# Performance work log

Hardware: AMD Instinct MI355X
Metric: run time of the kernel (lower is better)

## Reference

```python
import jax, jax.numpy as jnp
import numpy as np

N_NODES = 20000
N_EDGES = 320000
MUL = 64            # multiplicity of 0e and 1o in hidden/out irreps
NUM_BASIS = 8
INV_SQRT3 = 0.5773502691896258
EPS = 1e-5


def setup_inputs() -> dict:
    key = jax.random.key(0)
    k = jax.random.split(key, 16)
    return {
        "node_hiddens": jax.random.normal(k[0], (N_NODES, 4 * MUL), dtype=jnp.float32),
        "edge_attr": jax.random.uniform(k[1], (N_EDGES, NUM_BASIS), dtype=jnp.float32),
        "edge_sh": jax.random.normal(k[2], (N_EDGES, 4), dtype=jnp.float32),
        "w1_s": jax.random.normal(k[3], (MUL, MUL), dtype=jnp.float32),
        "w1_v": jax.random.normal(k[4], (MUL, MUL), dtype=jnp.float32),
        "wsc_s": jax.random.normal(k[5], (MUL, MUL), dtype=jnp.float32),
        "wsc_v": jax.random.normal(k[6], (MUL, MUL), dtype=jnp.float32),
        "w2_s": jax.random.normal(k[7], (2 * MUL, MUL), dtype=jnp.float32),
        "w2_v": jax.random.normal(k[8], (2 * MUL, MUL), dtype=jnp.float32),
        "fc_w1": jax.random.normal(k[9], (NUM_BASIS, 64), dtype=jnp.float32),
        "fc_w2": jax.random.normal(k[10], (64, 64), dtype=jnp.float32),
        "fc_w3": jax.random.normal(k[11], (64, 4 * MUL), dtype=jnp.float32),
        "g_s": jnp.ones((MUL,), dtype=jnp.float32),
        "g_v": jnp.ones((MUL,), dtype=jnp.float32),
        "edge_index": jax.random.randint(k[12], (2, N_EDGES), 0, N_NODES),
    }


def reference(node_hiddens, edge_attr, edge_sh, w1_s, w1_v, wsc_s, wsc_v,
              w2_s, w2_v, fc_w1, fc_w2, fc_w3, g_s, g_v, edge_index):
    N = node_hiddens.shape[0]
    # e3nn layout: [N, 64x0e | 64x1o] with mul-major vectors
    xs = node_hiddens[:, :MUL]                        # [N, 64]
    xv = node_hiddens[:, MUL:].reshape(N, MUL, 3)     # [N, 64, 3]

    # edge MLP (FullyConnectedNet([8,64,64,256], silu)) -> per-edge TP weights
    h = jax.nn.silu(edge_attr @ fc_w1 * (1.0 / np.sqrt(float(NUM_BASIS))))
    h = jax.nn.silu(h @ fc_w2 * (1.0 / np.sqrt(64.0)))
    w = h @ fc_w3 * (1.0 / np.sqrt(64.0))             # [E, 4*MUL]
    wA, wB, wC, wD = jnp.split(w, 4, axis=1)          # one 64-vec per uvu path

    inv = 1.0 / np.sqrt(float(MUL))
    # self-connection Linear(hidden -> out)
    sc_s = xs @ wsc_s * inv
    sc_v = jnp.einsum('nud,uv->nvd', xv, wsc_v) * inv
    # linear_1 Linear(hidden -> hidden)
    ys = xs @ w1_s * inv
    yv = jnp.einsum('nud,uv->nvd', xv, w1_v) * inv

    src = edge_index[0]
    dst = edge_index[1]
    es = ys[dst]                                      # [E, 64] gather
    ev = yv[dst]                                      # [E, 64, 3]
    sh0 = edge_sh[:, :1]                              # [E, 1]
    sh1 = edge_sh[:, 1:]                              # [E, 3]

    # weighted uvu Clebsch-Gordan tensor product -> irreps_mid (sorted order)
    m0a = wA * es * sh0                                          # 0e x 0e -> 0e
    m0b = wD * jnp.einsum('eud,ed->eu', ev, sh1) * INV_SQRT3     # 1o x 1o -> 0e
    m1a = wB[:, :, None] * es[:, :, None] * sh1[:, None, :]      # 0e x 1o -> 1o
    m1b = wC[:, :, None] * ev * sh0[:, :, None]                  # 1o x 0e -> 1o
    mid_s = jnp.concatenate([m0a, m0b], axis=1)       # [E, 128]
    mid_v = jnp.concatenate([m1a, m1b], axis=1)       # [E, 128, 3]

    # scatter-sum to source nodes + 1/sqrt(degree) normalization
    ns = jax.ops.segment_sum(mid_s, src, num_segments=N)
    nv = jax.ops.segment_sum(mid_v, src, num_segments=N)
    deg = jax.ops.segment_sum(jnp.ones((src.shape[0],), node_hiddens.dtype), src, num_segments=N)
    dn = jax.lax.rsqrt(jnp.maximum(deg, 1.0))
    ns = ns * dn[:, None]
    nv = nv * dn[:, None, None]

    # linear_2 Linear(128x0e+128x1o -> 64x0e+64x1o) + self connection
    inv2 = 1.0 / np.sqrt(2.0 * MUL)
    os_ = ns @ w2_s * inv2 + sc_s
    ov = jnp.einsum('nud,uv->nvd', nv, w2_v) * inv2 + sc_v

    # equivariant RMS layer norm per irrep type (centering=False)
    os_ = os_ * jax.lax.rsqrt(jnp.mean(os_ * os_, axis=1, keepdims=True) + EPS) * g_s
    rms_v = jax.lax.rsqrt(jnp.mean(ov * ov, axis=(1, 2))[:, None, None] + EPS)
    ov = ov * rms_v * g_v[None, :, None]

    return jnp.concatenate([os_, ov.reshape(N, 3 * MUL)], axis=1)
```

## Files before the change

kernel.cpp:

```cpp
#include <hip/hip_runtime.h>
#include <math.h>

#define N_NODES 20000
#define N_EDGES 320000
#define N_TILES 1250

typedef __attribute__((ext_vector_type(8))) short bf16x8;
typedef __attribute__((ext_vector_type(4))) float f32x4;
typedef __attribute__((ext_vector_type(2))) unsigned u32x2;
typedef __attribute__((ext_vector_type(4))) unsigned u32x4;

__device__ __forceinline__ float silu_f(float x) {
    return x / (1.0f + __expf(-x));
}
__device__ __forceinline__ short f2bf(float x) {
    union { float f; unsigned u; } v; v.f = x;
    unsigned r = (v.u + 0x7FFFu + ((v.u >> 16) & 1u)) >> 16;
    return (short)r;
}
__device__ __forceinline__ float blo(unsigned u) { return __uint_as_float(u << 16); }
__device__ __forceinline__ float bhi(unsigned u) { return __uint_as_float(u & 0xFFFF0000u); }
__device__ __forceinline__ unsigned cvt_pk(float lo, float hi) {
    unsigned r;
    asm("v_cvt_pk_bf16_f32 %0, %1, %2" : "=v"(r) : "v"(lo), "v"(hi));
    return r;
}
__device__ __forceinline__ float rlane(float v, int l) {
    return __uint_as_float(__builtin_amdgcn_readlane(__float_as_uint(v), l));
}
#define MFMA16(a, b, c) __builtin_amdgcn_mfma_f32_16x16x32_bf16((a), (b), (c), 0, 0, 0)

__global__ __launch_bounds__(256) void s_hist(const int* __restrict__ eidx,
                                              int* __restrict__ cnt) {
    const int e = blockIdx.x * 256 + threadIdx.x;
    if (e < N_EDGES) atomicAdd(&cnt[eidx[e]], 1);
}

__global__ __launch_bounds__(1024) void s_scan(int* __restrict__ cnt,
                                               int* __restrict__ start) {
    const int tid = threadIdx.x;
    const int base = tid * 20;
    int vals[20];
    int sum = 0;
    #pragma unroll
    for (int j = 0; j < 20; ++j) {
        const int i = base + j;
        const int v = (i < N_NODES) ? cnt[i] : 0;
        vals[j] = sum;
        sum += v;
    }
    const int lane = tid & 63, wv = tid >> 6;
    int x = sum;
    #pragma unroll
    for (int off = 1; off < 64; off <<= 1) {
        const int t = __shfl_up(x, off);
        if (lane >= off) x += t;
    }
    __shared__ int wtot[16];
    if (lane == 63) wtot[wv] = x;
    __syncthreads();
    int wpref = 0;
    for (int k = 0; k < wv; ++k) wpref += wtot[k];
    const int excl = wpref + x - sum;
    #pragma unroll
    for (int j = 0; j < 20; ++j) {
        const int i = base + j;
        if (i < N_NODES) {
            const int s = excl + vals[j];
            start[i] = s;
            cnt[i] = s;
        }
    }
    if (tid == 1023) start[N_NODES] = wpref + x;
}

__global__ __launch_bounds__(256) void s_scatter(const int* __restrict__ eidx,
                                                 const float* __restrict__ esh,
                                                 int* __restrict__ cursor,
                                                 int* __restrict__ perm,
                                                 int* __restrict__ dst_perm,
                                                 float* __restrict__ esh_perm) {
    const int e = blockIdx.x * 256 + threadIdx.x;
    if (e >= N_EDGES) return;
    const int src = eidx[e];
    const int pos = atomicAdd(&cursor[src], 1);
    perm[pos] = e;
    dst_perm[pos] = eidx[N_EDGES + e];
    *(float4*)(esh_perm + (size_t)pos * 4) = *(const float4*)(esh + (size_t)e * 4);
}

__global__ __launch_bounds__(256) void k_pack(
    const float* __restrict__ fcw1, const float* __restrict__ fcw2,
    const float* __restrict__ fcw3,
    const float* __restrict__ w1s, const float* __restrict__ wscs,
    const float* __restrict__ w1v, const float* __restrict__ wscv,
    const float* __restrict__ w2s, const float* __restrict__ w2v,
    short* __restrict__ w1A, short* __restrict__ w2A, short* __restrict__ w3A,
    short* __restrict__ wp1, short* __restrict__ wp2)
{
    const int tid = blockIdx.x * 256 + threadIdx.x;
    const int nthr = gridDim.x * 256;
    for (int i = tid; i < 4*64*8; i += nthr) {
        const int j = i & 7, lane = (i >> 3) & 63, t = i >> 9;
        const int k = (lane >> 4) * 8 + j, row = t*16 + (lane & 15);
        w1A[i] = (k < 8) ? f2bf(fcw1[k*64 + row]) : (short)0;
    }
    for (int i = tid; i < 8*64*8; i += nthr) {
        const int j = i & 7, lane = (i >> 3) & 63, kk = (i >> 9) & 1, t = i >> 10;
        const int k = kk*32 + (lane >> 4)*8 + j, row = t*16 + (lane & 15);
        w2A[i] = f2bf(fcw2[k*64 + row]);
    }
    for (int i = tid; i < 32*64*8; i += nthr) {
        const int j = i & 7, lane = (i >> 3) & 63, kk = (i >> 9) & 1, T = i >> 10;
        const int k = kk*32 + (lane >> 4)*8 + j, c = T*16 + (lane & 15);
        const float s = (c >= 192) ? 0.5773502691896258f : 1.0f;
        w3A[i] = f2bf(fcw3[(size_t)k*256 + c] * s);
    }
    for (int i = tid; i < 4096; i += nthr) {
        const int j = i & 7, lane = (i >> 3) & 63, kk = (i >> 9) & 1, vt = i >> 10;
        const int row = vt*16 + (lane & 15), k = kk*32 + (lane >> 4)*8 + j;
        wp1[i]         = f2bf(w1s [k*64 + row]);
        wp1[4096 + i]  = f2bf(wscs[k*64 + row]);
        wp1[8192 + i]  = f2bf(w1v [k*64 + row]);
        wp1[12288 + i] = f2bf(wscv[k*64 + row]);
    }
    for (int i = tid; i < 8192; i += nthr) {
        const int j = i & 7, lane = (i >> 3) & 63, kk = (i >> 9) & 3, vt = i >> 11;
        const int row = vt*16 + (lane & 15), k = kk*32 + (lane >> 4)*8 + j;
        const int r = (k & 1)*64 + (k >> 1);
        wp2[i]        = f2bf(w2s[r*64 + row]);
        wp2[8192 + i] = f2bf(w2v[r*64 + row]);
    }
}

__global__ __launch_bounds__(256) void k1_mfma(
    const float* __restrict__ nh, const short* __restrict__ wp1,
    short* __restrict__ ydata, short* __restrict__ scpack)
{
    const int lane = threadIdx.x & 63;
    const int tile = blockIdx.x * 4 + (threadIdx.x >> 6);
    if (tile >= N_TILES) return;
    const int l15 = lane & 15, lhi = lane >> 4;
    const int n = tile*16 + l15;
    const float* row = nh + (size_t)n * 256;
    const f32x4 zz = {0.f, 0.f, 0.f, 0.f};
    f32x4 acc[8][4];
    #pragma unroll
    for (int c = 0; c < 8; ++c)
        #pragma unroll
        for (int vt = 0; vt < 4; ++vt) acc[c][vt] = zz;

    #pragma unroll
    for (int kk = 0; kk < 2; ++kk) {
        const int k0 = kk*32 + lhi*8;
        const float4 s0 = *(const float4*)(row + k0);
        const float4 s1 = *(const float4*)(row + k0 + 4);
        float4 vv[6];
        #pragma unroll
        for (int q = 0; q < 6; ++q) vv[q] = *(const float4*)(row + 64 + 3*k0 + q*4);
        const float* vf = (const float*)vv;
        union { u32x4 u; bf16x8 v; } bs, b0, b1, b2;
        bs.u[0] = cvt_pk(s0.x, s0.y); bs.u[1] = cvt_pk(s0.z, s0.w);
        bs.u[2] = cvt_pk(s1.x, s1.y); bs.u[3] = cvt_pk(s1.z, s1.w);
        #pragma unroll
        for (int q = 0; q < 4; ++q) {
            b0.u[q] = cvt_pk(vf[6*q + 0], vf[6*q + 3]);
            b1.u[q] = cvt_pk(vf[6*q + 1], vf[6*q + 4]);
            b2.u[q] = cvt_pk(vf[6*q + 2], vf[6*q + 5]);
        }
        #pragma unroll
        for (int vt = 0; vt < 4; ++vt) {
            const int fo = ((vt*2 + kk)*64 + lane)*8;
            const bf16x8 a_ys = *(const bf16x8*)&wp1[fo];
            const bf16x8 a_ss = *(const bf16x8*)&wp1[4096 + fo];
            const bf16x8 a_yv = *(const bf16x8*)&wp1[8192 + fo];
            const bf16x8 a_sv = *(const bf16x8*)&wp1[12288 + fo];
            acc[0][vt] = MFMA16(a_ys, bs.v, acc[0][vt]);
            acc[1][vt] = MFMA16(a_ss, bs.v, acc[1][vt]);
            acc[2][vt] = MFMA16(a_yv, b0.v, acc[2][vt]);
            acc[3][vt] = MFMA16(a_yv, b1.v, acc[3][vt]);
            acc[4][vt] = MFMA16(a_yv, b2.v, acc[4][vt]);
            acc[5][vt] = MFMA16(a_sv, b0.v, acc[5][vt]);
            acc[6][vt] = MFMA16(a_sv, b1.v, acc[6][vt]);
            acc[7][vt] = MFMA16(a_sv, b2.v, acc[7][vt]);
        }
    }
    #pragma unroll
    for (int vt = 0; vt < 4; ++vt)
        #pragma unroll
        for (int r = 0; r < 4; ++r) {
            const int v = vt*16 + lhi*4 + r;
            u32x2 yo, so;
            yo[0] = cvt_pk(acc[0][vt][r]*0.125f, acc[2][vt][r]*0.125f);
            yo[1] = cvt_pk(acc[3][vt][r]*0.125f, acc[4][vt][r]*0.125f);
            so[0] = cvt_pk(acc[1][vt][r]*0.125f, acc[5][vt][r]*0.125f);
            so[1] = cvt_pk(acc[6][vt][r]*0.125f, acc[7][vt][r]*0.125f);
            *(u32x2*)&ydata [((size_t)n*64 + v)*4] = yo;
            *(u32x2*)&scpack[((size_t)n*64 + v)*4] = so;
        }
}

__global__ __launch_bounds__(256) void k_mlp(
    const float* __restrict__ ea, const int* __restrict__ perm,
    const short* __restrict__ w1A, const short* __restrict__ w2A,
    const short* __restrict__ w3A, short* __restrict__ wq)
{
    __shared__ short hb1[4][1024];
    __shared__ short hb2[4][1024];
    const int lane = threadIdx.x & 63, w = threadIdx.x >> 6;
    const int l15 = lane & 15, lhi = lane >> 4;
    const int wbase = (blockIdx.x * 4 + w) * 64;
    short* h1b = hb1[w];
    short* h2b = hb2[w];
    const int swz = (l15 & 7) << 4;
    const f32x4 zz = {0.f, 0.f, 0.f, 0.f};

    bf16x8 a1[4], a2[4][2];
    #pragma unroll
    for (int t = 0; t < 4; ++t)
        a1[t] = *(const bf16x8*)&w1A[(t*64 + lane)*8];
    #pragma unroll
    for (int t = 0; t < 4; ++t)
        #pragma unroll
        for (int kk = 0; kk < 2; ++kk)
            a2[t][kk] = *(const bf16x8*)&w2A[((t*2 + kk)*64 + lane)*8];

    bf16x8 bh2[4][2];
    for (int sb = 0; sb < 4; ++sb) {
        bf16x8 bea = {0,0,0,0,0,0,0,0};
        if (lhi == 0) {
            const int e = perm[wbase + sb*16 + l15];
            const float4 p0 = *(const float4*)(ea + (size_t)e*8);
            const float4 p1 = *(const float4*)(ea + (size_t)e*8 + 4);
            union { u32x4 u; bf16x8 v; } tu;
            tu.u[0] = cvt_pk(p0.x, p0.y);
            tu.u[1] = cvt_pk(p0.z, p0.w);
            tu.u[2] = cvt_pk(p1.x, p1.y);
            tu.u[3] = cvt_pk(p1.z, p1.w);
            bea = tu.v;
        }
        f32x4 d1[4];
        #pragma unroll
        for (int t = 0; t < 4; ++t)
            d1[t] = MFMA16(a1[t], bea, zz);
        #pragma unroll
        for (int t = 0; t < 4; ++t) {
            const float s0 = silu_f(d1[t][0] * 0.35355339059327373f);
            const float s1 = silu_f(d1[t][1] * 0.35355339059327373f);
            const float s2 = silu_f(d1[t][2] * 0.35355339059327373f);
            const float s3 = silu_f(d1[t][3] * 0.35355339059327373f);
            u32x2 pk; pk[0] = cvt_pk(s0, s1); pk[1] = cvt_pk(s2, s3);
            const int byt = (l15*128 + t*32 + lhi*8) ^ swz;
            *(u32x2*)((char*)h1b + byt) = pk;
        }
        bf16x8 bh1[2];
        #pragma unroll
        for (int kk = 0; kk < 2; ++kk)
            bh1[kk] = *(const bf16x8*)((const char*)h1b + ((l15*128 + kk*64 + lhi*16) ^ swz));
        f32x4 d2[4];
        #pragma unroll
        for (int t = 0; t < 4; ++t) {
            d2[t] = MFMA16(a2[t][0], bh1[0], zz);
            d2[t] = MFMA16(a2[t][1], bh1[1], d2[t]);
        }
        #pragma unroll
        for (int t = 0; t < 4; ++t) {
            const float s0 = silu_f(d2[t][0] * 0.125f) * 0.125f;
            const float s1 = silu_f(d2[t][1] * 0.125f) * 0.125f;
            const float s2 = silu_f(d2[t][2] * 0.125f) * 0.125f;
            const float s3 = silu_f(d2[t][3] * 0.125f) * 0.125f;
            u32x2 pk; pk[0] = cvt_pk(s0, s1); pk[1] = cvt_pk(s2, s3);
            const int byt = (l15*128 + t*32 + lhi*8) ^ swz;
            *(u32x2*)((char*)h2b + byt) = pk;
        }
        #pragma unroll
        for (int kk = 0; kk < 2; ++kk)
            bh2[sb][kk] = *(const bf16x8*)((const char*)h2b + ((l15*128 + kk*64 + lhi*16) ^ swz));
    }

    #pragma unroll
    for (int c = 0; c < 4; ++c) {
        f32x4 dq[4][4];
        #pragma unroll
        for (int q = 0; q < 4; ++q) {
            const int T = q*4 + c;
            const bf16x8 a30 = *(const bf16x8*)&w3A[((T*2 + 0)*64 + lane)*8];
            const bf16x8 a31 = *(const bf16x8*)&w3A[((T*2 + 1)*64 + lane)*8];
            #pragma unroll
            for (int sb = 0; sb < 4; ++sb) {
                f32x4 d = MFMA16(a30, bh2[sb][0], zz);
                dq[q][sb] = MFMA16(a31, bh2[sb][1], d);
            }
        }
        #pragma unroll
        for (int sb = 0; sb < 4; ++sb) {
            const int slot = wbase + sb*16 + l15;
            #pragma unroll
            for (int r = 0; r < 4; ++r) {
                const int v = c*16 + lhi*4 + r;
                u32x2 pk;
                pk[0] = cvt_pk(dq[0][sb][r], dq[1][sb][r]);
                pk[1] = cvt_pk(dq[2][sb][r], dq[3][sb][r]);
                *(u32x2*)&wq[((size_t)slot*64 + v)*4] = pk;
            }
        }
    }
}

__global__ __launch_bounds__(256) void k2_gather(
    const int* __restrict__ start, const int* __restrict__ dst_perm,
    const float* __restrict__ esh_perm, const short* __restrict__ wq,
    const short* __restrict__ ydata, unsigned* __restrict__ ncat32)
{
    const int lane = threadIdx.x & 63;
    const int n = blockIdx.x * 4 + (threadIdx.x >> 6);
    if (n >= N_NODES) return;
    const int s0 = start[n], s1 = start[n + 1];
    float acc0=0.f, acc1=0.f, av0=0.f, av1=0.f, av2=0.f, bv0=0.f, bv1=0.f, bv2=0.f;
    for (int p = s0; p < s1; p += 8) {
        const int m = s1 - p;
        u32x2 wv[8], yd[8];
        float4 sh[8];
        #pragma unroll
        for (int j = 0; j < 8; ++j) {
            const int pp = (j < m) ? p + j : s0;
            wv[j] = *(const u32x2*)&wq[((size_t)pp*64 + lane)*4];
            sh[j] = *(const float4*)(esh_perm + (size_t)pp*4);
            const int dst = dst_perm[pp];
            yd[j] = *(const u32x2*)&ydata[((size_t)dst*64 + lane)*4];
        }
        #pragma unroll
        for (int j = 0; j < 8; ++j) {
            const float g = (j < m) ? 1.f : 0.f;
            const float wa = blo(wv[j][0])*g, wb = bhi(wv[j][0])*g;
            const float wc = blo(wv[j][1])*g, wd = bhi(wv[j][1])*g;
            const float es  = blo(yd[j][0]), ev0 = bhi(yd[j][0]);
            const float ev1 = blo(yd[j][1]), ev2 = bhi(yd[j][1]);
            acc0 += wa * es * sh[j].x;
            acc1 += wd * (ev0*sh[j].y + ev1*sh[j].z + ev2*sh[j].w);
            const float esb = wb * es;
            av0 += esb * sh[j].y; av1 += esb * sh[j].z; av2 += esb * sh[j].w;
            const float c0 = wc * sh[j].x;
            bv0 += c0 * ev0; bv1 += c0 * ev1; bv2 += c0 * ev2;
        }
    }
    unsigned* nrow = ncat32 + (size_t)n * 256;
    nrow[lane]        = cvt_pk(acc0, acc1);
    nrow[64  + lane]  = cvt_pk(av0, bv0);
    nrow[128 + lane]  = cvt_pk(av1, bv1);
    nrow[192 + lane]  = cvt_pk(av2, bv2);
}

__global__ __launch_bounds__(256) void k2_seg(
    const float* __restrict__ ea, const float* __restrict__ esh_perm,
    const int* __restrict__ perm, const int* __restrict__ dst_perm,
    const int* __restrict__ start,
    const float* __restrict__ fcw1, const float* __restrict__ fcw2,
    const float* __restrict__ fcw3,
    const short* __restrict__ ydata, unsigned* __restrict__ ncat32)
{
    __shared__ float lw1[8*64];
    __shared__ float lw2[64*64];
    for (int i = threadIdx.x; i < 8*64; i += 256)  lw1[i] = fcw1[i];
    for (int i = threadIdx.x; i < 64*64; i += 256) lw2[i] = fcw2[i];
    __syncthreads();
    const int lane = threadIdx.x & 63;
    const int n = blockIdx.x * 4 + (threadIdx.x >> 6);
    if (n >= N_NODES) return;
    const int s0 = start[n], s1 = start[n + 1];
    float acc0=0.f, acc1=0.f, av0=0.f, av1=0.f, av2=0.f, bv0=0.f, bv1=0.f, bv2=0.f;
    for (int p = s0; p < s1; p += 4) {
        int idx[4];
        float h1[4];
        #pragma unroll
        for (int j = 0; j < 4; ++j) {
            const bool ok = (p + j < s1);
            idx[j] = ok ? p + j : p;
            const float* eap = ea + (size_t)perm[idx[j]] * 8;
            float a = 0.f;
            #pragma unroll
            for (int u = 0; u < 8; ++u) a += eap[u] * lw1[u*64 + lane];
            a = ok ? a * 0.35355339059327373f : 0.f;
            h1[j] = silu_f(a);
        }
        float h2[4] = {0.f, 0.f, 0.f, 0.f};
        #pragma unroll 8
        for (int u = 0; u < 64; ++u) {
            const float wv = lw2[u*64 + lane];
            h2[0] += rlane(h1[0], u) * wv;
            h2[1] += rlane(h1[1], u) * wv;
            h2[2] += rlane(h1[2], u) * wv;
            h2[3] += rlane(h1[3], u) * wv;
        }
        #pragma unroll
        for (int j = 0; j < 4; ++j) h2[j] = silu_f(h2[j] * 0.125f) * 0.125f;
        float wa[4] = {0,0,0,0}, wb[4] = {0,0,0,0}, wc[4] = {0,0,0,0}, wd[4] = {0,0,0,0};
        #pragma unroll 4
        for (int u = 0; u < 64; ++u) {
            const float* r = fcw3 + u * 256;
            const float r0 = r[lane], r1 = r[64 + lane], r2 = r[128 + lane], r3 = r[192 + lane];
            #pragma unroll
            for (int j = 0; j < 4; ++j) {
                const float hu = rlane(h2[j], u);
                wa[j] += hu * r0; wb[j] += hu * r1; wc[j] += hu * r2; wd[j] += hu * r3;
            }
        }
        #pragma unroll
        for (int j = 0; j < 4; ++j) {
            const int pp = idx[j];
            const float4 sh = *(const float4*)(esh_perm + (size_t)pp*4);
            const int dst = dst_perm[pp];
            const u32x2 yd = *(const u32x2*)&ydata[((size_t)dst*64 + lane)*4];
            const float es  = blo(yd[0]), ev0 = bhi(yd[0]);
            const float ev1 = blo(yd[1]), ev2 = bhi(yd[1]);
            acc0 += wa[j] * es * sh.x;
            acc1 += wd[j] * (ev0*sh.y + ev1*sh.z + ev2*sh.w) * 0.5773502691896258f;
            const float esb = wb[j] * es;
            av0 += esb * sh.y; av1 += esb * sh.z; av2 += esb * sh.w;
            const float c0 = wc[j] * sh.x;
            bv0 += c0 * ev0; bv1 += c0 * ev1; bv2 += c0 * ev2;
        }
    }
    unsigned* nrow = ncat32 + (size_t)n * 256;
    nrow[lane]        = cvt_pk(acc0, acc1);
    nrow[64  + lane]  = cvt_pk(av0, bv0);
    nrow[128 + lane]  = cvt_pk(av1, bv1);
    nrow[192 + lane]  = cvt_pk(av2, bv2);
}

__global__ __launch_bounds__(256) void k3_mfma(
    const unsigned* __restrict__ ncat32, const int* __restrict__ start,
    const short* __restrict__ wp2, const short* __restrict__ scpack,
    const float* __restrict__ gs, const float* __restrict__ gv,
    float* __restrict__ out)
{
    const int lane = threadIdx.x & 63;
    const int tile = blockIdx.x * 4 + (threadIdx.x >> 6);
    if (tile >= N_TILES) return;
    const int l15 = lane & 15, lhi = lane >> 4;
    const int n = tile*16 + l15;
    const f32x4 zz = {0.f, 0.f, 0.f, 0.f};
    f32x4 acc[4][4];
    #pragma unroll
    for (int c = 0; c < 4; ++c)
        #pragma unroll
        for (int vt = 0; vt < 4; ++vt) acc[c][vt] = zz;

    const size_t nb = (size_t)n * 256;
    #pragma unroll
    for (int kk = 0; kk < 4; ++kk) {
        const int uo = kk*16 + lhi*4;
        union { u32x4 u; bf16x8 v; } bs, b0, b1, b2;
        bs.u = *(const u32x4*)&ncat32[nb +        uo];
        b0.u = *(const u32x4*)&ncat32[nb +  64 + uo];
        b1.u = *(const u32x4*)&ncat32[nb + 128 + uo];
        b2.u = *(const u32x4*)&ncat32[nb + 192 + uo];
        #pragma unroll
        for (int vt = 0; vt < 4; ++vt) {
            const int fo = ((vt*4 + kk)*64 + lane)*8;
            const bf16x8 a_s = *(const bf16x8*)&wp2[fo];
            const bf16x8 a_v = *(const bf16x8*)&wp2[8192 + fo];
            acc[0][vt] = MFMA16(a_s, bs.v, acc[0][vt]);
            acc[1][vt] = MFMA16(a_v, b0.v, acc[1][vt]);
            acc[2][vt] = MFMA16(a_v, b1.v, acc[2][vt]);
            acc[3][vt] = MFMA16(a_v, b2.v, acc[3][vt]);
        }
    }
    const float degf = (float)(start[n+1] - start[n]);
    const float coef = rsqrtf(fmaxf(degf, 1.0f)) * 0.08838834764831845f;
    float os[4][4], o0[4][4], o1[4][4], o2[4][4];
    float ssq = 0.f, vsq = 0.f;
    #pragma unroll
    for (int vt = 0; vt < 4; ++vt)
        #pragma unroll
        for (int r = 0; r < 4; ++r) {
            const int v = vt*16 + lhi*4 + r;
            const u32x2 sc = *(const u32x2*)&scpack[((size_t)n*64 + v)*4];
            os[vt][r] = acc[0][vt][r]*coef + blo(sc[0]);
            o0[vt][r] = acc[1][vt][r]*coef + bhi(sc[0]);
            o1[vt][r] = acc[2][vt][r]*coef + blo(sc[1]);
            o2[vt][r] = acc[3][vt][r]*coef + bhi(sc[1]);
            ssq += os[vt][r]*os[vt][r];
            vsq += o0[vt][r]*o0[vt][r] + o1[vt][r]*o1[vt][r] + o2[vt][r]*o2[vt][r];
        }
    ssq += __shfl_xor(ssq, 16); ssq += __shfl_xor(ssq, 32);
    vsq += __shfl_xor(vsq, 16); vsq += __shfl_xor(vsq, 32);
    const float rs = rsqrtf(ssq * (1.0f/64.0f) + 1e-5f);
    const float rv = rsqrtf(vsq * (1.0f/192.0f) + 1e-5f);
    float* orow = out + (size_t)n * 256;
    #pragma unroll
    for (int vt = 0; vt < 4; ++vt) {
        const int vb = vt*16 + lhi*4;
        const float4 g4  = *(const float4*)(gs + vb);
        const float4 gv4 = *(const float4*)(gv + vb);
        const float4 so = { os[vt][0]*rs*g4.x, os[vt][1]*rs*g4.y,
                            os[vt][2]*rs*g4.z, os[vt][3]*rs*g4.w };
        *(float4*)(orow + vb) = so;
        const float m0 = rv*gv4.x, m1 = rv*gv4.y, m2 = rv*gv4.z, m3 = rv*gv4.w;
        const float4 w0 = { o0[vt][0]*m0, o1[vt][0]*m0, o2[vt][0]*m0, o0[vt][1]*m1 };
        const float4 w1 = { o1[vt][1]*m1, o2[vt][1]*m1, o0[vt][2]*m2, o1[vt][2]*m2 };
        const float4 w2 = { o2[vt][2]*m2, o0[vt][3]*m3, o1[vt][3]*m3, o2[vt][3]*m3 };
        float* vbase = orow + 64 + vb*3;
        *(float4*)(vbase)     = w0;
        *(float4*)(vbase + 4) = w1;
        *(float4*)(vbase + 8) = w2;
    }
}

extern "C" void kernel_launch(void* const* d_in, const int* in_sizes, int n_in,
                              void* d_out, int out_size, void* d_ws, size_t ws_size,
                              hipStream_t stream) {
    const float* nh   = (const float*)d_in[0];
    const float* ea   = (const float*)d_in[1];
    const float* esh  = (const float*)d_in[2];
    const float* w1s  = (const float*)d_in[3];
    const float* w1v  = (const float*)d_in[4];
    const float* wscs = (const float*)d_in[5];
    const float* wscv = (const float*)d_in[6];
    const float* w2s  = (const float*)d_in[7];
    const float* w2v  = (const float*)d_in[8];
    const float* fcw1 = (const float*)d_in[9];
    const float* fcw2 = (const float*)d_in[10];
    const float* fcw3 = (const float*)d_in[11];
    const float* gs   = (const float*)d_in[12];
    const float* gv   = (const float*)d_in[13];
    const int*   eidx = (const int*)d_in[14];
    float* out = (float*)d_out;

    char* wsb = (char*)d_ws;
    size_t off = 0;
    short* ydata  = (short*)(wsb + off); off += (size_t)N_NODES * 256 * 2;
    short* scpack = (short*)(wsb + off); off += (size_t)N_NODES * 256 * 2;
    unsigned* ncat32 = (unsigned*)(wsb + off); off += (size_t)N_NODES * 256 * 4;
    float* esh_perm  = (float*)(wsb + off); off += (size_t)N_EDGES * 4 * 4;
    int* cnt      = (int*)(wsb + off); off += (size_t)N_NODES * 4;
    int* start    = (int*)(wsb + off); off += ((size_t)N_NODES + 1) * 4;
    int* perm     = (int*)(wsb + off); off += (size_t)N_EDGES * 4;
    int* dst_perm = (int*)(wsb + off); off += (size_t)N_EDGES * 4;
    short* w1A = (short*)(wsb + off); off += 2048 * 2;
    short* w2A = (short*)(wsb + off); off += 4096 * 2;
    short* w3A = (short*)(wsb + off); off += 16384 * 2;
    short* wp1 = (short*)(wsb + off); off += 16384 * 2;
    short* wp2 = (short*)(wsb + off); off += 16384 * 2;
    off = (off + 15) & ~(size_t)15;
    short* wq = (short*)(wsb + off);
    const size_t need = off + (size_t)N_EDGES * 256 * 2;

    hipMemsetAsync(cnt, 0, N_NODES * sizeof(int), stream);

    s_hist<<<(N_EDGES + 255)/256, 256, 0, stream>>>(eidx, cnt);
    s_scan<<<1, 1024, 0, stream>>>(cnt, start);
    s_scatter<<<(N_EDGES + 255)/256, 256, 0, stream>>>(
        eidx, esh, cnt, perm, dst_perm, esh_perm);

    k_pack<<<32, 256, 0, stream>>>(fcw1, fcw2, fcw3, w1s, wscs, w1v, wscv,
                                   w2s, w2v, w1A, w2A, w3A, wp1, wp2);

    k1_mfma<<<(N_TILES + 3)/4, 256, 0, stream>>>(nh, wp1, ydata, scpack);

    if (ws_size >= need) {
        k_mlp<<<N_EDGES/256, 256, 0, stream>>>(ea, perm, w1A, w2A, w3A, wq);
        k2_gather<<<(N_NODES + 3)/4, 256, 0, stream>>>(
            start, dst_perm, esh_perm, wq, ydata, ncat32);
    } else {
        k2_seg<<<(N_NODES + 3)/4, 256, 0, stream>>>(
            ea, esh_perm, perm, dst_perm, start, fcw1, fcw2, fcw3, ydata, ncat32);
    }

    k3_mfma<<<(N_TILES + 3)/4, 256, 0, stream>>>(
        ncat32, start, wp2, scpack, gs, gv, out);
}
```

Before: 227.6 us.

## Fuse edge MLP with message gather and segmented atomic reduction

```diff
diff --git a/kernel.cpp b/kernel.cpp
--- a/kernel.cpp
+++ b/kernel.cpp
@@ -25,9 +25,6 @@
     asm("v_cvt_pk_bf16_f32 %0, %1, %2" : "=v"(r) : "v"(lo), "v"(hi));
     return r;
 }
-__device__ __forceinline__ float rlane(float v, int l) {
-    return __uint_as_float(__builtin_amdgcn_readlane(__float_as_uint(v), l));
-}
 #define MFMA16(a, b, c) __builtin_amdgcn_mfma_f32_16x16x32_bf16((a), (b), (c), 0, 0, 0)
 
 __global__ __launch_bounds__(256) void s_hist(const int* __restrict__ eidx,
@@ -79,6 +76,7 @@
                                                  int* __restrict__ cursor,
                                                  int* __restrict__ perm,
                                                  int* __restrict__ dst_perm,
+                                                 int* __restrict__ node_perm,
                                                  float* __restrict__ esh_perm) {
     const int e = blockIdx.x * 256 + threadIdx.x;
     if (e >= N_EDGES) return;
@@ -86,6 +84,7 @@
     const int pos = atomicAdd(&cursor[src], 1);
     perm[pos] = e;
     dst_perm[pos] = eidx[N_EDGES + e];
+    node_perm[pos] = src;
     *(float4*)(esh_perm + (size_t)pos * 4) = *(const float4*)(esh + (size_t)e * 4);
 }
 
@@ -127,9 +126,8 @@
     for (int i = tid; i < 8192; i += nthr) {
         const int j = i & 7, lane = (i >> 3) & 63, kk = (i >> 9) & 3, vt = i >> 11;
         const int row = vt*16 + (lane & 15), k = kk*32 + (lane >> 4)*8 + j;
-        const int r = (k & 1)*64 + (k >> 1);
-        wp2[i]        = f2bf(w2s[r*64 + row]);
-        wp2[8192 + i] = f2bf(w2v[r*64 + row]);
+        wp2[i]        = f2bf(w2s[k*64 + row]);
+        wp2[8192 + i] = f2bf(w2v[k*64 + row]);
     }
 }
 
@@ -200,18 +198,23 @@
         }
 }
 
-__global__ __launch_bounds__(256) void k_mlp(
+__global__ __launch_bounds__(256) void k_msg(
     const float* __restrict__ ea, const int* __restrict__ perm,
+    const int* __restrict__ dst_perm, const int* __restrict__ node_perm,
+    const int* __restrict__ start, const float* __restrict__ esh_perm,
     const short* __restrict__ w1A, const short* __restrict__ w2A,
-    const short* __restrict__ w3A, short* __restrict__ wq)
+    const short* __restrict__ w3A, const short* __restrict__ ydata,
+    float* __restrict__ ncat)
 {
     __shared__ short hb1[4][1024];
     __shared__ short hb2[4][1024];
+    __shared__ short wslab[4][4096];
     const int lane = threadIdx.x & 63, w = threadIdx.x >> 6;
     const int l15 = lane & 15, lhi = lane >> 4;
     const int wbase = (blockIdx.x * 4 + w) * 64;
     short* h1b = hb1[w];
     short* h2b = hb2[w];
+    short* slab = wslab[w];
     const int swz = (l15 & 7) << 4;
     const f32x4 zz = {0.f, 0.f, 0.f, 0.f};
 
@@ -225,7 +228,25 @@
         for (int kk = 0; kk < 2; ++kk)
             a2[t][kk] = *(const bf16x8*)&w2A[((t*2 + kk)*64 + lane)*8];
 
-    bf16x8 bh2[4][2];
+    int cur = node_perm[wbase];
+    int s_lo = start[cur], s_hi = start[cur + 1];
+    float acc0=0.f, acc1=0.f, av0=0.f, av1=0.f, av2=0.f, bv0=0.f, bv1=0.f, bv2=0.f;
+
+    auto flushfn = [&]() {
+        float* b = ncat + ((size_t)cur*64 + lane)*8;
+        if (s_lo >= wbase && s_hi <= wbase + 64) {
+            const float4 x0 = { acc0, av0, av1, av2 };
+            const float4 x1 = { acc1, bv0, bv1, bv2 };
+            *(float4*)b = x0;
+            *(float4*)(b + 4) = x1;
+        } else {
+            atomicAdd(b + 0, acc0); atomicAdd(b + 1, av0);
+            atomicAdd(b + 2, av1); atomicAdd(b + 3, av2);
+            atomicAdd(b + 4, acc1); atomicAdd(b + 5, bv0);
+            atomicAdd(b + 6, bv1); atomicAdd(b + 7, bv2);
+        }
+    };
+
     for (int sb = 0; sb < 4; ++sb) {
         bf16x8 bea = {0,0,0,0,0,0,0,0};
         if (lhi == 0) {
@@ -273,163 +294,58 @@
             const int byt = (l15*128 + t*32 + lhi*8) ^ swz;
             *(u32x2*)((char*)h2b + byt) = pk;
         }
+        bf16x8 bh2[2];
         #pragma unroll
         for (int kk = 0; kk < 2; ++kk)
-            bh2[sb][kk] = *(const bf16x8*)((const char*)h2b + ((l15*128 + kk*64 + lhi*16) ^ swz));
-    }
-
-    #pragma unroll
-    for (int c = 0; c < 4; ++c) {
-        f32x4 dq[4][4];
-        #pragma unroll
-        for (int q = 0; q < 4; ++q) {
-            const int T = q*4 + c;
+            bh2[kk] = *(const bf16x8*)((const char*)h2b + ((l15*128 + kk*64 + lhi*16) ^ swz));
+
+        #pragma unroll
+        for (int T = 0; T < 16; ++T) {
             const bf16x8 a30 = *(const bf16x8*)&w3A[((T*2 + 0)*64 + lane)*8];
             const bf16x8 a31 = *(const bf16x8*)&w3A[((T*2 + 1)*64 + lane)*8];
-            #pragma unroll
-            for (int sb = 0; sb < 4; ++sb) {
-                f32x4 d = MFMA16(a30, bh2[sb][0], zz);
-                dq[q][sb] = MFMA16(a31, bh2[sb][1], d);
+            f32x4 d = MFMA16(a30, bh2[0], zz);
+            d = MFMA16(a31, bh2[1], d);
+            const int g = T >> 2;
+            const int vb = (T & 3)*16 + lhi*4;
+            const unsigned p01 = cvt_pk(d[0], d[1]);
+            const unsigned p23 = cvt_pk(d[2], d[3]);
+            short* sl = slab + l15*256;
+            const int m = l15 & 7;
+            sl[(((vb + 0) ^ m) << 2) + g] = (short)(p01 & 0xFFFFu);
+            sl[(((vb + 1) ^ m) << 2) + g] = (short)(p01 >> 16);
+            sl[(((vb + 2) ^ m) << 2) + g] = (short)(p23 & 0xFFFFu);
+            sl[(((vb + 3) ^ m) << 2) + g] = (short)(p23 >> 16);
+        }
+
+        for (int i = 0; i < 16; ++i) {
+            const int slot = wbase + sb*16 + i;
+            if (slot >= s_hi) {
+                flushfn();
+                cur = node_perm[slot];
+                s_lo = start[cur]; s_hi = start[cur + 1];
+                acc0=0.f; acc1=0.f; av0=0.f; av1=0.f; av2=0.f; bv0=0.f; bv1=0.f; bv2=0.f;
             }
-        }
-        #pragma unroll
-        for (int sb = 0; sb < 4; ++sb) {
-            const int slot = wbase + sb*16 + l15;
-            #pragma unroll
-            for (int r = 0; r < 4; ++r) {
-                const int v = c*16 + lhi*4 + r;
-                u32x2 pk;
-                pk[0] = cvt_pk(dq[0][sb][r], dq[1][sb][r]);
-                pk[1] = cvt_pk(dq[2][sb][r], dq[3][sb][r]);
-                *(u32x2*)&wq[((size_t)slot*64 + v)*4] = pk;
-            }
-        }
-    }
-}
-
-__global__ __launch_bounds__(256) void k2_gather(
-    const int* __restrict__ start, const int* __restrict__ dst_perm,
-    const float* __restrict__ esh_perm, const short* __restrict__ wq,
-    const short* __restrict__ ydata, unsigned* __restrict__ ncat32)
-{
-    const int lane = threadIdx.x & 63;
-    const int n = blockIdx.x * 4 + (threadIdx.x >> 6);
-    if (n >= N_NODES) return;
-    const int s0 = start[n], s1 = start[n + 1];
-    float acc0=0.f, acc1=0.f, av0=0.f, av1=0.f, av2=0.f, bv0=0.f, bv1=0.f, bv2=0.f;
-    for (int p = s0; p < s1; p += 8) {
-        const int m = s1 - p;
-        u32x2 wv[8], yd[8];
-        float4 sh[8];
-        #pragma unroll
-        for (int j = 0; j < 8; ++j) {
-            const int pp = (j < m) ? p + j : s0;
-            wv[j] = *(const u32x2*)&wq[((size_t)pp*64 + lane)*4];
-            sh[j] = *(const float4*)(esh_perm + (size_t)pp*4);
-            const int dst = dst_perm[pp];
-            yd[j] = *(const u32x2*)&ydata[((size_t)dst*64 + lane)*4];
-        }
-        #pragma unroll
-        for (int j = 0; j < 8; ++j) {
-            const float g = (j < m) ? 1.f : 0.f;
-            const float wa = blo(wv[j][0])*g, wb = bhi(wv[j][0])*g;
-            const float wc = blo(wv[j][1])*g, wd = bhi(wv[j][1])*g;
-            const float es  = blo(yd[j][0]), ev0 = bhi(yd[j][0]);
-            const float ev1 = blo(yd[j][1]), ev2 = bhi(yd[j][1]);
-            acc0 += wa * es * sh[j].x;
-            acc1 += wd * (ev0*sh[j].y + ev1*sh[j].z + ev2*sh[j].w);
-            const float esb = wb * es;
-            av0 += esb * sh[j].y; av1 += esb * sh[j].z; av2 += esb * sh[j].w;
-            const float c0 = wc * sh[j].x;
-            bv0 += c0 * ev0; bv1 += c0 * ev1; bv2 += c0 * ev2;
-        }
-    }
-    unsigned* nrow = ncat32 + (size_t)n * 256;
-    nrow[lane]        = cvt_pk(acc0, acc1);
-    nrow[64  + lane]  = cvt_pk(av0, bv0);
-    nrow[128 + lane]  = cvt_pk(av1, bv1);
-    nrow[192 + lane]  = cvt_pk(av2, bv2);
-}
-
-__global__ __launch_bounds__(256) void k2_seg(
-    const float* __restrict__ ea, const float* __restrict__ esh_perm,
-    const int* __restrict__ perm, const int* __restrict__ dst_perm,
-    const int* __restrict__ start,
-    const float* __restrict__ fcw1, const float* __restrict__ fcw2,
-    const float* __restrict__ fcw3,
-    const short* __restrict__ ydata, unsigned* __restrict__ ncat32)
-{
-    __shared__ float lw1[8*64];
-    __shared__ float lw2[64*64];
-    for (int i = threadIdx.x; i < 8*64; i += 256)  lw1[i] = fcw1[i];
-    for (int i = threadIdx.x; i < 64*64; i += 256) lw2[i] = fcw2[i];
-    __syncthreads();
-    const int lane = threadIdx.x & 63;
-    const int n = blockIdx.x * 4 + (threadIdx.x >> 6);
-    if (n >= N_NODES) return;
-    const int s0 = start[n], s1 = start[n + 1];
-    float acc0=0.f, acc1=0.f, av0=0.f, av1=0.f, av2=0.f, bv0=0.f, bv1=0.f, bv2=0.f;
-    for (int p = s0; p < s1; p += 4) {
-        int idx[4];
-        float h1[4];
-        #pragma unroll
-        for (int j = 0; j < 4; ++j) {
-            const bool ok = (p + j < s1);
-            idx[j] = ok ? p + j : p;
-            const float* eap = ea + (size_t)perm[idx[j]] * 8;
-            float a = 0.f;
-            #pragma unroll
-            for (int u = 0; u < 8; ++u) a += eap[u] * lw1[u*64 + lane];
-            a = ok ? a * 0.35355339059327373f : 0.f;
-            h1[j] = silu_f(a);
-        }
-        float h2[4] = {0.f, 0.f, 0.f, 0.f};
-        #pragma unroll 8
-        for (int u = 0; u < 64; ++u) {
-            const float wv = lw2[u*64 + lane];
-            h2[0] += rlane(h1[0], u) * wv;
-            h2[1] += rlane(h1[1], u) * wv;
-            h2[2] += rlane(h1[2], u) * wv;
-            h2[3] += rlane(h1[3], u) * wv;
-        }
-        #pragma unroll
-        for (int j = 0; j < 4; ++j) h2[j] = silu_f(h2[j] * 0.125f) * 0.125f;
-        float wa[4] = {0,0,0,0}, wb[4] = {0,0,0,0}, wc[4] = {0,0,0,0}, wd[4] = {0,0,0,0};
-        #pragma unroll 4
-        for (int u = 0; u < 64; ++u) {
-            const float* r = fcw3 + u * 256;
-            const float r0 = r[lane], r1 = r[64 + lane], r2 = r[128 + lane], r3 = r[192 + lane];
-            #pragma unroll
-            for (int j = 0; j < 4; ++j) {
-                const float hu = rlane(h2[j], u);
-                wa[j] += hu * r0; wb[j] += hu * r1; wc[j] += hu * r2; wd[j] += hu * r3;
-            }
-        }
-        #pragma unroll
-        for (int j = 0; j < 4; ++j) {
-            const int pp = idx[j];
-            const float4 sh = *(const float4*)(esh_perm + (size_t)pp*4);
-            const int dst = dst_perm[pp];
+            const u32x2 wv = *(const u32x2*)(slab + i*256 + ((lane ^ (i & 7)) << 2));
+            const int dst = dst_perm[slot];
+            const float4 sh = *(const float4*)(esh_perm + (size_t)slot*4);
             const u32x2 yd = *(const u32x2*)&ydata[((size_t)dst*64 + lane)*4];
+            const float wa = blo(wv[0]), wb = bhi(wv[0]);
+            const float wc = blo(wv[1]), wd = bhi(wv[1]);
             const float es  = blo(yd[0]), ev0 = bhi(yd[0]);
             const float ev1 = blo(yd[1]), ev2 = bhi(yd[1]);
-            acc0 += wa[j] * es * sh.x;
-            acc1 += wd[j] * (ev0*sh.y + ev1*sh.z + ev2*sh.w) * 0.5773502691896258f;
-            const float esb = wb[j] * es;
+            acc0 += wa * es * sh.x;
+            acc1 += wd * (ev0*sh.y + ev1*sh.z + ev2*sh.w);
+            const float esb = wb * es;
             av0 += esb * sh.y; av1 += esb * sh.z; av2 += esb * sh.w;
-            const float c0 = wc[j] * sh.x;
+            const float c0 = wc * sh.x;
             bv0 += c0 * ev0; bv1 += c0 * ev1; bv2 += c0 * ev2;
         }
     }
-    unsigned* nrow = ncat32 + (size_t)n * 256;
-    nrow[lane]        = cvt_pk(acc0, acc1);
-    nrow[64  + lane]  = cvt_pk(av0, bv0);
-    nrow[128 + lane]  = cvt_pk(av1, bv1);
-    nrow[192 + lane]  = cvt_pk(av2, bv2);
+    flushfn();
 }
 
 __global__ __launch_bounds__(256) void k3_mfma(
-    const unsigned* __restrict__ ncat32, const int* __restrict__ start,
+    const float* __restrict__ ncat, const int* __restrict__ start,
     const short* __restrict__ wp2, const short* __restrict__ scpack,
     const float* __restrict__ gs, const float* __restrict__ gv,
     float* __restrict__ out)
@@ -446,15 +362,22 @@
         #pragma unroll
         for (int vt = 0; vt < 4; ++vt) acc[c][vt] = zz;
 
-    const size_t nb = (size_t)n * 256;
     #pragma unroll
     for (int kk = 0; kk < 4; ++kk) {
-        const int uo = kk*16 + lhi*4;
+        const int u0 = (kk & 1)*32 + lhi*8;
+        const int c = (kk >> 1)*4;
+        float4 ld[8];
+        #pragma unroll
+        for (int j = 0; j < 8; ++j)
+            ld[j] = *(const float4*)(ncat + ((size_t)n*64 + u0 + j)*8 + c);
         union { u32x4 u; bf16x8 v; } bs, b0, b1, b2;
-        bs.u = *(const u32x4*)&ncat32[nb +        uo];
-        b0.u = *(const u32x4*)&ncat32[nb +  64 + uo];
-        b1.u = *(const u32x4*)&ncat32[nb + 128 + uo];
-        b2.u = *(const u32x4*)&ncat32[nb + 192 + uo];
+        #pragma unroll
+        for (int q = 0; q < 4; ++q) {
+            bs.u[q] = cvt_pk(ld[2*q].x, ld[2*q+1].x);
+            b0.u[q] = cvt_pk(ld[2*q].y, ld[2*q+1].y);
+            b1.u[q] = cvt_pk(ld[2*q].z, ld[2*q+1].z);
+            b2.u[q] = cvt_pk(ld[2*q].w, ld[2*q+1].w);
+        }
         #pragma unroll
         for (int vt = 0; vt < 4; ++vt) {
             const int fo = ((vt*4 + kk)*64 + lane)*8;
@@ -531,42 +454,36 @@
     size_t off = 0;
     short* ydata  = (short*)(wsb + off); off += (size_t)N_NODES * 256 * 2;
     short* scpack = (short*)(wsb + off); off += (size_t)N_NODES * 256 * 2;
-    unsigned* ncat32 = (unsigned*)(wsb + off); off += (size_t)N_NODES * 256 * 4;
-    float* esh_perm  = (float*)(wsb + off); off += (size_t)N_EDGES * 4 * 4;
-    int* cnt      = (int*)(wsb + off); off += (size_t)N_NODES * 4;
-    int* start    = (int*)(wsb + off); off += ((size_t)N_NODES + 1) * 4;
-    int* perm     = (int*)(wsb + off); off += (size_t)N_EDGES * 4;
-    int* dst_perm = (int*)(wsb + off); off += (size_t)N_EDGES * 4;
+    float* ncat   = (float*)(wsb + off); off += (size_t)N_NODES * 512 * 4;
+    float* esh_perm = (float*)(wsb + off); off += (size_t)N_EDGES * 4 * 4;
+    int* cnt       = (int*)(wsb + off); off += (size_t)N_NODES * 4;
+    int* start     = (int*)(wsb + off); off += ((size_t)N_NODES + 1) * 4;
+    int* perm      = (int*)(wsb + off); off += (size_t)N_EDGES * 4;
+    int* dst_perm  = (int*)(wsb + off); off += (size_t)N_EDGES * 4;
+    int* node_perm = (int*)(wsb + off); off += (size_t)N_EDGES * 4;
     short* w1A = (short*)(wsb + off); off += 2048 * 2;
     short* w2A = (short*)(wsb + off); off += 4096 * 2;
     short* w3A = (short*)(wsb + off); off += 16384 * 2;
     short* wp1 = (short*)(wsb + off); off += 16384 * 2;
     short* wp2 = (short*)(wsb + off); off += 16384 * 2;
-    off = (off + 15) & ~(size_t)15;
-    short* wq = (short*)(wsb + off);
-    const size_t need = off + (size_t)N_EDGES * 256 * 2;
 
     hipMemsetAsync(cnt, 0, N_NODES * sizeof(int), stream);
+    hipMemsetAsync(ncat, 0, (size_t)N_NODES * 512 * sizeof(float), stream);
 
     s_hist<<<(N_EDGES + 255)/256, 256, 0, stream>>>(eidx, cnt);
     s_scan<<<1, 1024, 0, stream>>>(cnt, start);
     s_scatter<<<(N_EDGES + 255)/256, 256, 0, stream>>>(
-        eidx, esh, cnt, perm, dst_perm, esh_perm);
+        eidx, esh, cnt, perm, dst_perm, node_perm, esh_perm);
 
     k_pack<<<32, 256, 0, stream>>>(fcw1, fcw2, fcw3, w1s, wscs, w1v, wscv,
                                    w2s, w2v, w1A, w2A, w3A, wp1, wp2);
 
     k1_mfma<<<(N_TILES + 3)/4, 256, 0, stream>>>(nh, wp1, ydata, scpack);
 
-    if (ws_size >= need) {
-        k_mlp<<<N_EDGES/256, 256, 0, stream>>>(ea, perm, w1A, w2A, w3A, wq);
-        k2_gather<<<(N_NODES + 3)/4, 256, 0, stream>>>(
-            start, dst_perm, esh_perm, wq, ydata, ncat32);
-    } else {
-        k2_seg<<<(N_NODES + 3)/4, 256, 0, stream>>>(
-            ea, esh_perm, perm, dst_perm, start, fcw1, fcw2, fcw3, ydata, ncat32);
-    }
+    k_msg<<<N_EDGES/256, 256, 0, stream>>>(
+        ea, perm, dst_perm, node_perm, start, esh_perm,
+        w1A, w2A, w3A, ydata, ncat);
 
     k3_mfma<<<(N_TILES + 3)/4, 256, 0, stream>>>(
-        ncat32, start, wp2, scpack, gs, gv, out);
-}
+        ncat, start, wp2, scpack, gs, gv, out);
+}
```

Result: slower. 351.1 us (+54.3%).
